# Kernel tuning notes

Measured on AMD Instinct MI355X. Metric: run time of the kernel, lower is better.

Reference implementation:

```python
import jax, jax.numpy as jnp
import numpy as np

N_NODES = 100000
N_EDGES = 400000
IN_DIM, HID, OUT_DIM, NUM_REL = 768, 256, 128, 3


def _init_linear(key, fan_in, fan_out):
    k1, k2 = jax.random.split(key)
    s = 1.0 / np.sqrt(fan_in)
    W = jax.random.uniform(k1, (fan_in, fan_out), jnp.float32, -s, s)
    b = jax.random.uniform(k2, (fan_out,), jnp.float32, -s, s)
    return W, b


def setup_inputs() -> dict:
    key = jax.random.key(0)
    ks = jax.random.split(key, 12)
    x = jax.random.normal(ks[0], (N_NODES, IN_DIM), jnp.float32)
    edge_index = jax.random.randint(ks[1], (2, N_EDGES), 0, N_NODES, jnp.int64 if jax.config.jax_enable_x64 else jnp.int32).astype(jnp.int32)
    edge_type = jax.random.randint(ks[2], (N_EDGES,), 0, NUM_REL).astype(jnp.int32)
    W1, b1 = _init_linear(ks[3], IN_DIM, HID)
    s = 1.0 / np.sqrt(HID)
    conv1_W = jax.random.uniform(ks[4], (NUM_REL, HID, HID), jnp.float32, -s, s)
    conv1_root = jax.random.uniform(ks[5], (HID, HID), jnp.float32, -s, s)
    conv1_bias = jnp.zeros((HID,), jnp.float32)
    conv2_W = jax.random.uniform(ks[6], (NUM_REL, HID, HID), jnp.float32, -s, s)
    conv2_root = jax.random.uniform(ks[7], (HID, HID), jnp.float32, -s, s)
    conv2_bias = jnp.zeros((HID,), jnp.float32)
    W2, b2 = _init_linear(ks[8], HID, OUT_DIM)
    Wc, bc = _init_linear(ks[9], OUT_DIM, 2)
    return {"x": x, "edge_index": edge_index, "edge_type": edge_type,
            "batch_size": 1024,
            "W1": W1, "b1": b1,
            "conv1_W": conv1_W, "conv1_root": conv1_root, "conv1_bias": conv1_bias,
            "conv2_W": conv2_W, "conv2_root": conv2_root, "conv2_bias": conv2_bias,
            "W2": W2, "b2": b2, "Wc": Wc, "bc": bc}


def rgcn_conv(h, src, dst, edge_type, W, root, bias):
    # PyG RGCNConv: mean aggregation per relation + root transform + bias
    n = h.shape[0]
    hs = h[src]                                   # [E, HID] gather
    out = h @ root + bias                         # root/self term
    for r in range(NUM_REL):                      # fixed small relation count
        w = (edge_type == r).astype(h.dtype)      # [E]
        msg = (hs @ W[r]) * w[:, None]            # per-relation transform
        ssum = jax.ops.segment_sum(msg, dst, num_segments=n)
        cnt = jax.ops.segment_sum(w, dst, num_segments=n)
        out = out + ssum / jnp.maximum(cnt, 1.0)[:, None]
    return out


def reference(x, edge_index, edge_type, batch_size,
              W1, b1, conv1_W, conv1_root, conv1_bias,
              conv2_W, conv2_root, conv2_bias, W2, b2, Wc, bc):
    src, dst = edge_index[0], edge_index[1]
    h = jax.nn.relu(x @ W1 + b1)                  # linear1 + ReLU
    h = rgcn_conv(h, src, dst, edge_type, conv1_W, conv1_root, conv1_bias)
    # dropout: identity at inference
    h = rgcn_conv(h, src, dst, edge_type, conv2_W, conv2_root, conv2_bias)
    h = jax.nn.relu(h @ W2 + b2)                  # linear2 + ReLU
    logits = h @ Wc + bc                          # classifier
    return logits[:batch_size]
```

## Files before the change

kernel.cpp:

```cpp
#include <hip/hip_runtime.h>


#define N_NODES 100000
#define N_EDGES 400000
#define IN_DIM  768
#define HID     256
#define OUT_DIM 128
#define NREL    3
#define BATCH   1024
#define KCAT    1024
#define MSGW    768
#define CAP0    32768
#define CAP1    8192
#define ECAP1   32768
#define ECAP2   8192

typedef __attribute__((ext_vector_type(8))) short bf16x8;
typedef __attribute__((ext_vector_type(4))) float f32x4;

static __device__ __forceinline__ int imin(int a, int b) { return a < b ? a : b; }

static __device__ __forceinline__ unsigned short f2bf(float f) {
    union { float f; unsigned int u; } v; v.f = f;
    unsigned int r = v.u + 0x7FFFu + ((v.u >> 16) & 1u);
    return (unsigned short)(r >> 16);
}

#define P1n  ((IN_DIM * HID) / 8)
#define P2n  ((KCAT * HID) / 8)
#define PW2n ((HID * OUT_DIM) / 8)

__global__ __launch_bounds__(256) void prep_mark1(
    uint4* __restrict__ zp, int nzA,
    const float* __restrict__ W1,
    const float* __restrict__ c1root, const float* __restrict__ c1W,
    const float* __restrict__ c2root, const float* __restrict__ c2W,
    const float* __restrict__ W2,
    unsigned short* __restrict__ w1s,
    unsigned short* __restrict__ B1s,
    unsigned short* __restrict__ B2s,
    unsigned short* __restrict__ W2t,
    const int* __restrict__ ei, int* __restrict__ need1,
    int* __restrict__ elist2, int* __restrict__ ectr2)
{
    int t = blockIdx.x * blockDim.x + threadIdx.x;
    if (t < nzA) { zp[t] = make_uint4(0u, 0u, 0u, 0u); return; }
    int u = t - nzA;
    if (u < P1n) {
        int base = u * 8;
        int j0 = base & 31, c = (base >> 5) & 255, s = base >> 13;
        unsigned int pk[4];
        #pragma unroll
        for (int q = 0; q < 4; q++) {
            unsigned short lo = f2bf(W1[((s * 32 + j0 + 2 * q) << 8) + c]);
            unsigned short hi = f2bf(W1[((s * 32 + j0 + 2 * q + 1) << 8) + c]);
            pk[q] = (unsigned int)lo | ((unsigned int)hi << 16);
        }
        *(uint4*)&w1s[base] = make_uint4(pk[0], pk[1], pk[2], pk[3]);
        return;
    }
    u -= P1n;
    if (u < 2 * P2n) {
        int which2 = u >= P2n;
        const float* root = which2 ? c2root : c1root;
        const float* Wr   = which2 ? c2W : c1W;
        unsigned short* dst = which2 ? B2s : B1s;
        int base = (u - (which2 ? P2n : 0)) * 8;
        int j0 = base & 31, c = (base >> 5) & 255, s = base >> 13;
        int k0 = s * 32 + j0;
        unsigned int pk[4];
        #pragma unroll
        for (int q = 0; q < 4; q++) {
            int ka = k0 + 2 * q, kb = ka + 1;
            float va = (ka < HID) ? root[(ka << 8) + c] : Wr[((ka - HID) << 8) + c];
            float vb = (kb < HID) ? root[(kb << 8) + c] : Wr[((kb - HID) << 8) + c];
            pk[q] = (unsigned int)f2bf(va) | ((unsigned int)f2bf(vb) << 16);
        }
        *(uint4*)&dst[base] = make_uint4(pk[0], pk[1], pk[2], pk[3]);
        return;
    }
    u -= 2 * P2n;
    if (u < PW2n) {
        int s = u >> 9, f = (u >> 6) & 7, l = u & 63;
        int kb = s * 32 + ((l >> 4) << 3);
        int c  = (f << 4) + (l & 15);
        unsigned int pk[4];
        #pragma unroll
        for (int q = 0; q < 4; q++) {
            unsigned short lo = f2bf(W2[(size_t)(kb + 2 * q)     * OUT_DIM + c]);
            unsigned short hi = f2bf(W2[(size_t)(kb + 2 * q + 1) * OUT_DIM + c]);
            pk[q] = (unsigned int)lo | ((unsigned int)hi << 16);
        }
        *(uint4*)&W2t[(size_t)u * 8] = make_uint4(pk[0], pk[1], pk[2], pk[3]);
        return;
    }
    u -= PW2n;
    if (u < N_EDGES) {
        if (ei[N_EDGES + u] < BATCH) {
            need1[ei[u]] = 1;
            int p = atomicAdd(ectr2, 1);
            if (p < ECAP2) elist2[p] = u;
        }
    }
}

__global__ void mark0_compact1(const int* __restrict__ ei, const int* __restrict__ need1,
                               int* __restrict__ need0,
                               int* __restrict__ elist1, int* __restrict__ ectr1,
                               int* __restrict__ idx1, int* __restrict__ map1,
                               int* __restrict__ n1ctr) {
    int t = blockIdx.x * blockDim.x + threadIdx.x;
    if (t < N_EDGES) {
        int d = ei[N_EDGES + t];
        if (d < BATCH || need1[d]) {
            need0[ei[t]] = 1;
            int p = atomicAdd(ectr1, 1);
            if (p < ECAP1) elist1[p] = t;
        }
        return;
    }
    int i = t - N_EDGES;
    if (i < N_NODES) {
        if ((i < BATCH) | need1[i]) {
            int p = atomicAdd(n1ctr, 1);
            if (p < CAP1) { idx1[p] = i; map1[i] = p; } else map1[i] = -1;
        } else map1[i] = -1;
    }
}

__global__ void compact0(const int* __restrict__ map1, const int* __restrict__ need0,
                         int* __restrict__ idx0, int* __restrict__ map0,
                         int* __restrict__ n0ctr) {
    int i = blockIdx.x * blockDim.x + threadIdx.x;
    if (i >= N_NODES) return;
    if ((map1[i] >= 0) | need0[i]) {
        int p = atomicAdd(n0ctr, 1);
        if (p < CAP0) { idx0[p] = i; map0[i] = p; } else map0[i] = -1;
    } else map0[i] = -1;
}

__global__ void scatter_c(const int* __restrict__ ei, const int* __restrict__ et,
                          const int* __restrict__ elist, const int* __restrict__ ectr, int ecap,
                          const int* __restrict__ mapSrc, const int* __restrict__ mapDst,
                          const float* __restrict__ hsrc,
                          float* __restrict__ Amsg, float* __restrict__ cnt,
                          int cntStride) {
    int g = blockIdx.x * blockDim.x + threadIdx.x;
    int ii = g >> 6, lane = g & 63;
    int n = imin(*ectr, ecap);
    if (ii >= n) return;
    int e = elist[ii];
    int d = ei[N_EDGES + e];
    int row = mapDst ? mapDst[d] : d;
    if (row < 0) return;
    int s = mapSrc[ei[e]];
    if (s < 0) return;
    int r = et[e];
    float4 v = *(const float4*)(hsrc + (size_t)s * HID + lane * 4);
    float* dp = Amsg + (size_t)row * MSGW + (size_t)r * HID + lane * 4;
    atomicAdd(dp + 0, v.x);
    atomicAdd(dp + 1, v.y);
    atomicAdd(dp + 2, v.z);
    atomicAdd(dp + 3, v.w);
    if (lane == 0) atomicAdd(cnt + (size_t)r * cntStride + row, 1.0f);
}

__global__ __launch_bounds__(256) void gemm1_mfma(
    const float* __restrict__ x, const int* __restrict__ idx0,
    const unsigned short* __restrict__ w1s, const float* __restrict__ b1,
    float* __restrict__ h0c, const int* __restrict__ Mptr, int Mcap)
{
    int M = imin(*Mptr, Mcap);
    int bm = blockIdx.x * 64;
    if (bm >= M) return;

    __shared__ unsigned short As[64][40];
    __shared__ unsigned short Bs[256][40];

    int tid = threadIdx.x;
    int w = tid >> 6, lane = tid & 63;
    int l16 = lane & 15, lhi = lane >> 4;

    int ar = tid >> 2, ac = tid & 3;
    int gr = idx0[imin(bm + ar, M - 1)];
    const float* aptr = x + (size_t)gr * IN_DIM + ac * 8;

    f32x4 acc[16];
    #pragma unroll
    for (int i = 0; i < 16; i++) acc[i] = (f32x4)0.0f;

    for (int k0 = 0; k0 < IN_DIM; k0 += 32) {
        float4 a0 = *(const float4*)(aptr + k0);
        float4 a1 = *(const float4*)(aptr + k0 + 4);
        unsigned int p0 = (unsigned int)f2bf(a0.x) | ((unsigned int)f2bf(a0.y) << 16);
        unsigned int p1 = (unsigned int)f2bf(a0.z) | ((unsigned int)f2bf(a0.w) << 16);
        unsigned int p2 = (unsigned int)f2bf(a1.x) | ((unsigned int)f2bf(a1.y) << 16);
        unsigned int p3 = (unsigned int)f2bf(a1.z) | ((unsigned int)f2bf(a1.w) << 16);
        *(uint4*)&As[ar][ac * 8] = make_uint4(p0, p1, p2, p3);

        const uint4* bsrc = (const uint4*)(w1s + ((size_t)(k0 >> 5) * 256 + tid) * 32);
        int bswz = (tid >> 3) & 3;
        uint4 b0 = bsrc[0], b1v = bsrc[1], b2 = bsrc[2], b3 = bsrc[3];
        *(uint4*)&Bs[tid][(0 ^ bswz) * 8] = b0;
        *(uint4*)&Bs[tid][(1 ^ bswz) * 8] = b1v;
        *(uint4*)&Bs[tid][(2 ^ bswz) * 8] = b2;
        *(uint4*)&Bs[tid][(3 ^ bswz) * 8] = b3;
        __syncthreads();

        bf16x8 af = *(bf16x8*)&As[w * 16 + l16][lhi * 8];
        #pragma unroll
        for (int f = 0; f < 16; f++) {
            int col = f * 16 + l16;
            bf16x8 bf = *(bf16x8*)&Bs[col][(lhi ^ ((col >> 3) & 3)) * 8];
            acc[f] = __builtin_amdgcn_mfma_f32_16x16x32_bf16(af, bf, acc[f], 0, 0, 0);
        }
        __syncthreads();
    }

    #pragma unroll
    for (int f = 0; f < 16; f++) {
        int col = f * 16 + l16;
        float bb = b1[col];
        #pragma unroll
        for (int reg = 0; reg < 4; reg++) {
            int row = bm + w * 16 + lhi * 4 + reg;
            if (row < M) h0c[(size_t)row * HID + col] = fmaxf(acc[f][reg] + bb, 0.0f);
        }
    }
}

__global__ __launch_bounds__(256) void conv_mfma(
    const float* __restrict__ hsrc,
    const int* __restrict__ idx, const int* __restrict__ map,
    const float* __restrict__ Amsg,
    const float* __restrict__ cnt, int cntStride,
    const unsigned short* __restrict__ Bt, const float* __restrict__ bias,
    float* __restrict__ Cout, const int* __restrict__ Mptr, int Mcap)
{
    int M = Mptr ? imin(*Mptr, Mcap) : Mcap;
    int bm = blockIdx.x * 64;
    if (bm >= M) return;

    __shared__ unsigned short As[64][40];
    __shared__ unsigned short Bs[256][40];

    int tid = threadIdx.x;
    int w = tid >> 6, lane = tid & 63;
    int l16 = lane & 15, lhi = lane >> 4;

    int ar = tid >> 2, ac = tid & 3;
    int row = imin(bm + ar, M - 1);
    int node = idx ? idx[row] : row;
    int grow = map[node]; if (grow < 0) grow = 0;
    const float* rootp = hsrc + (size_t)grow * HID + ac * 8;
    const float* msgp  = Amsg + (size_t)row * MSGW + ac * 8;
    float sc[NREL];
    #pragma unroll
    for (int r = 0; r < NREL; r++)
        sc[r] = 1.0f / fmaxf(cnt[(size_t)r * cntStride + row], 1.0f);

    f32x4 acc[16];
    #pragma unroll
    for (int i = 0; i < 16; i++) acc[i] = (f32x4)0.0f;

    for (int k0 = 0; k0 < KCAT; k0 += 32) {
        float4 a0, a1;
        if (k0 < HID) {
            a0 = *(const float4*)(rootp + k0);
            a1 = *(const float4*)(rootp + k0 + 4);
        } else {
            float s = sc[(k0 - HID) >> 8];
            a0 = *(const float4*)(msgp + (k0 - HID));
            a1 = *(const float4*)(msgp + (k0 - HID) + 4);
            a0.x *= s; a0.y *= s; a0.z *= s; a0.w *= s;
            a1.x *= s; a1.y *= s; a1.z *= s; a1.w *= s;
        }
        unsigned int p0 = (unsigned int)f2bf(a0.x) | ((unsigned int)f2bf(a0.y) << 16);
        unsigned int p1 = (unsigned int)f2bf(a0.z) | ((unsigned int)f2bf(a0.w) << 16);
        unsigned int p2 = (unsigned int)f2bf(a1.x) | ((unsigned int)f2bf(a1.y) << 16);
        unsigned int p3 = (unsigned int)f2bf(a1.z) | ((unsigned int)f2bf(a1.w) << 16);
        *(uint4*)&As[ar][ac * 8] = make_uint4(p0, p1, p2, p3);

        const uint4* bsrc = (const uint4*)(Bt + ((size_t)(k0 >> 5) * 256 + tid) * 32);
        int bswz = (tid >> 3) & 3;
        uint4 b0 = bsrc[0], b1v = bsrc[1], b2 = bsrc[2], b3 = bsrc[3];
        *(uint4*)&Bs[tid][(0 ^ bswz) * 8] = b0;
        *(uint4*)&Bs[tid][(1 ^ bswz) * 8] = b1v;
        *(uint4*)&Bs[tid][(2 ^ bswz) * 8] = b2;
        *(uint4*)&Bs[tid][(3 ^ bswz) * 8] = b3;
        __syncthreads();

        bf16x8 af = *(bf16x8*)&As[w * 16 + l16][lhi * 8];
        #pragma unroll
        for (int f = 0; f < 16; f++) {
            int col = f * 16 + l16;
            bf16x8 bf = *(bf16x8*)&Bs[col][(lhi ^ ((col >> 3) & 3)) * 8];
            acc[f] = __builtin_amdgcn_mfma_f32_16x16x32_bf16(af, bf, acc[f], 0, 0, 0);
        }
        __syncthreads();
    }

    #pragma unroll
    for (int f = 0; f < 16; f++) {
        int col = f * 16 + l16;
        float bb = bias[col];
        #pragma unroll
        for (int reg = 0; reg < 4; reg++) {
            int r = bm + w * 16 + lhi * 4 + reg;
            if (r < M) Cout[(size_t)r * HID + col] = acc[f][reg] + bb;
        }
    }
}

__global__ __launch_bounds__(256) void conv2_fused(
    const float* __restrict__ hsrc, const int* __restrict__ map,
    const float* __restrict__ Amsg, const float* __restrict__ cnt,
    const unsigned short* __restrict__ Bt, const float* __restrict__ c2bias,
    const unsigned short* __restrict__ W2t, const float* __restrict__ b2,
    const float* __restrict__ Wc, const float* __restrict__ bc,
    float* __restrict__ out)
{
    int bm = blockIdx.x * 64;

    __shared__ unsigned short As[64][40];
    __shared__ unsigned short Bs[256][40];
    __shared__ unsigned short h2s[64][264];

    int tid = threadIdx.x;
    int w = tid >> 6, lane = tid & 63;
    int l16 = lane & 15, lhi = lane >> 4;

    int ar = tid >> 2, ac = tid & 3;
    int row = bm + ar;
    int grow = map[row]; if (grow < 0) grow = 0;
    const float* rootp = hsrc + (size_t)grow * HID + ac * 8;
    const float* msgp  = Amsg + (size_t)row * MSGW + ac * 8;
    float sc[NREL];
    #pragma unroll
    for (int r = 0; r < NREL; r++)
        sc[r] = 1.0f / fmaxf(cnt[(size_t)r * BATCH + row], 1.0f);

    f32x4 acc[16];
    #pragma unroll
    for (int i = 0; i < 16; i++) acc[i] = (f32x4)0.0f;

    for (int k0 = 0; k0 < KCAT; k0 += 32) {
        float4 a0, a1;
        if (k0 < HID) {
            a0 = *(const float4*)(rootp + k0);
            a1 = *(const float4*)(rootp + k0 + 4);
        } else {
            float s = sc[(k0 - HID) >> 8];
            a0 = *(const float4*)(msgp + (k0 - HID));
            a1 = *(const float4*)(msgp + (k0 - HID) + 4);
            a0.x *= s; a0.y *= s; a0.z *= s; a0.w *= s;
            a1.x *= s; a1.y *= s; a1.z *= s; a1.w *= s;
        }
        unsigned int p0 = (unsigned int)f2bf(a0.x) | ((unsigned int)f2bf(a0.y) << 16);
        unsigned int p1 = (unsigned int)f2bf(a0.z) | ((unsigned int)f2bf(a0.w) << 16);
        unsigned int p2 = (unsigned int)f2bf(a1.x) | ((unsigned int)f2bf(a1.y) << 16);
        unsigned int p3 = (unsigned int)f2bf(a1.z) | ((unsigned int)f2bf(a1.w) << 16);
        *(uint4*)&As[ar][ac * 8] = make_uint4(p0, p1, p2, p3);

        const uint4* bsrc = (const uint4*)(Bt + ((size_t)(k0 >> 5) * 256 + tid) * 32);
        int bswz = (tid >> 3) & 3;
        uint4 b0 = bsrc[0], b1v = bsrc[1], b2v = bsrc[2], b3 = bsrc[3];
        *(uint4*)&Bs[tid][(0 ^ bswz) * 8] = b0;
        *(uint4*)&Bs[tid][(1 ^ bswz) * 8] = b1v;
        *(uint4*)&Bs[tid][(2 ^ bswz) * 8] = b2v;
        *(uint4*)&Bs[tid][(3 ^ bswz) * 8] = b3;
        __syncthreads();

        bf16x8 af = *(bf16x8*)&As[w * 16 + l16][lhi * 8];
        #pragma unroll
        for (int f = 0; f < 16; f++) {
            int col = f * 16 + l16;
            bf16x8 bf = *(bf16x8*)&Bs[col][(lhi ^ ((col >> 3) & 3)) * 8];
            acc[f] = __builtin_amdgcn_mfma_f32_16x16x32_bf16(af, bf, acc[f], 0, 0, 0);
        }
        __syncthreads();
    }

    #pragma unroll
    for (int f = 0; f < 16; f++) {
        int col = f * 16 + l16;
        float bb = c2bias[col];
        #pragma unroll
        for (int reg = 0; reg < 4; reg++)
            h2s[w * 16 + lhi * 4 + reg][col] = f2bf(acc[f][reg] + bb);
    }
    __syncthreads();

    f32x4 acc2[8];
    #pragma unroll
    for (int i = 0; i < 8; i++) acc2[i] = (f32x4)0.0f;
    for (int s = 0; s < 8; s++) {
        bf16x8 af = *(bf16x8*)&h2s[w * 16 + l16][s * 32 + lhi * 8];
        #pragma unroll
        for (int f = 0; f < 8; f++) {
            bf16x8 bf = *(const bf16x8*)(W2t + ((size_t)(s * 8 + f) * 64 + lane) * 8);
            acc2[f] = __builtin_amdgcn_mfma_f32_16x16x32_bf16(af, bf, acc2[f], 0, 0, 0);
        }
    }

    float p0[4] = {0.f, 0.f, 0.f, 0.f}, p1[4] = {0.f, 0.f, 0.f, 0.f};
    #pragma unroll
    for (int f = 0; f < 8; f++) {
        int col = f * 16 + l16;
        float w0 = Wc[col * 2 + 0], w1 = Wc[col * 2 + 1];
        float bb = b2[col];
        #pragma unroll
        for (int reg = 0; reg < 4; reg++) {
            float h = fmaxf(acc2[f][reg] + bb, 0.0f);
            p0[reg] += h * w0;
            p1[reg] += h * w1;
        }
    }
    #pragma unroll
    for (int o = 1; o <= 8; o <<= 1) {
        #pragma unroll
        for (int reg = 0; reg < 4; reg++) {
            p0[reg] += __shfl_xor(p0[reg], o);
            p1[reg] += __shfl_xor(p1[reg], o);
        }
    }
    if (l16 == 0) {
        #pragma unroll
        for (int reg = 0; reg < 4; reg++) {
            int r = bm + w * 16 + lhi * 4 + reg;
            out[r * 2 + 0] = p0[reg] + bc[0];
            out[r * 2 + 1] = p1[reg] + bc[1];
        }
    }
}


extern "C" void kernel_launch(void* const* d_in, const int* in_sizes, int n_in,
                              void* d_out, int out_size, void* d_ws, size_t ws_size,
                              hipStream_t stream) {
    const float* x      = (const float*)d_in[0];
    const int*   ei     = (const int*)d_in[1];
    const int*   et     = (const int*)d_in[2];
    const float* W1     = (const float*)d_in[4];
    const float* b1     = (const float*)d_in[5];
    const float* c1W    = (const float*)d_in[6];
    const float* c1root = (const float*)d_in[7];
    const float* c1bias = (const float*)d_in[8];
    const float* c2W    = (const float*)d_in[9];
    const float* c2root = (const float*)d_in[10];
    const float* c2bias = (const float*)d_in[11];
    const float* W2     = (const float*)d_in[12];
    const float* b2     = (const float*)d_in[13];
    const float* Wc     = (const float*)d_in[14];
    const float* bc     = (const float*)d_in[15];
    float* out = (float*)d_out;

    char* ws = (char*)d_ws;
    size_t off = 0;
    auto alloc = [&](size_t bytes) -> char* {
        char* p = ws + off;
        off = (off + bytes + 255) & ~(size_t)255;
        return p;
    };

    size_t zb_ctr  = 16;
    size_t zb_cnt1 = (size_t)NREL * CAP1 * 4;
    size_t zb_cnt2 = (size_t)NREL * BATCH * 4;
    size_t zb_need = (size_t)N_NODES * 4;
    size_t msbytes = zb_ctr + zb_cnt1 + zb_cnt2 + 2 * zb_need;
    char* zsmall = alloc(msbytes);
    int*   n1ctr = (int*)zsmall;
    int*   n0ctr = n1ctr + 1;
    int*   ectr1 = n1ctr + 2;
    int*   ectr2 = n1ctr + 3;
    float* cnt1  = (float*)(zsmall + zb_ctr);
    float* cnt2  = (float*)(zsmall + zb_ctr + zb_cnt1);
    int*   need1 = (int*)(zsmall + zb_ctr + zb_cnt1 + zb_cnt2);
    int*   need0 = (int*)((char*)need1 + zb_need);

    size_t zb_amsg1 = (size_t)CAP1 * MSGW * 4;
    size_t zb_amsg2 = (size_t)BATCH * MSGW * 4;
    char* amsg = alloc(zb_amsg1 + zb_amsg2);
    float* Amsg1 = (float*)amsg;
    float* Amsg2 = (float*)(amsg + zb_amsg1);
    int nzA = (int)((zb_amsg1 + zb_amsg2) / 16);

    int* map1  = (int*)alloc(N_NODES * 4);
    int* map0  = (int*)alloc(N_NODES * 4);
    int* idx1  = (int*)alloc(CAP1 * 4);
    int* idx0  = (int*)alloc(CAP0 * 4);
    int* elist1 = (int*)alloc(ECAP1 * 4);
    int* elist2 = (int*)alloc(ECAP2 * 4);
    float* h0c = (float*)alloc((size_t)CAP0 * HID * 4);
    float* h1c = (float*)alloc((size_t)CAP1 * HID * 4);
    unsigned short* w1s = (unsigned short*)alloc((size_t)IN_DIM * HID * 2);
    unsigned short* B1s = (unsigned short*)alloc((size_t)KCAT * HID * 2);
    unsigned short* B2s = (unsigned short*)alloc((size_t)KCAT * HID * 2);
    unsigned short* W2t = (unsigned short*)alloc((size_t)HID * OUT_DIM * 2);
    (void)ws_size; (void)in_sizes; (void)n_in; (void)out_size;

    const int NB = 256;

    hipMemsetAsync(zsmall, 0, msbytes, stream);
    int n1_total = nzA + P1n + 2 * P2n + PW2n + N_EDGES;
    prep_mark1<<<dim3((n1_total + NB - 1) / NB), NB, 0, stream>>>(
        (uint4*)amsg, nzA, W1, c1root, c1W, c2root, c2W, W2,
        w1s, B1s, B2s, W2t, ei, need1, elist2, ectr2);
    int n2_total = N_EDGES + N_NODES;
    mark0_compact1<<<dim3((n2_total + NB - 1) / NB), NB, 0, stream>>>(
        ei, need1, need0, elist1, ectr1, idx1, map1, n1ctr);
    compact0<<<dim3((N_NODES + NB - 1) / NB), NB, 0, stream>>>(map1, need0, idx0, map0, n0ctr);
    gemm1_mfma<<<dim3(CAP0 / 64), NB, 0, stream>>>(x, idx0, w1s, b1, h0c, n0ctr, CAP0);
    scatter_c<<<dim3(ECAP1 * 64 / NB), NB, 0, stream>>>(ei, et, elist1, ectr1, ECAP1,
                                                        map0, map1, h0c, Amsg1, cnt1, CAP1);
    conv_mfma<<<dim3(CAP1 / 64), NB, 0, stream>>>(h0c, idx1, map0, Amsg1, cnt1, CAP1,
                                                  B1s, c1bias, h1c, n1ctr, CAP1);
    scatter_c<<<dim3(ECAP2 * 64 / NB), NB, 0, stream>>>(ei, et, elist2, ectr2, ECAP2,
                                                        map1, nullptr, h1c, Amsg2, cnt2, BATCH);
    conv2_fused<<<dim3(BATCH / 64), NB, 0, stream>>>(h1c, map1, Amsg2, cnt2,
                                                     B2s, c2bias, W2t, b2, Wc, bc, out);
}
```

Before: 379.4 us.

## Fuse layer-2 scatter into conv1 epilogue via per-tile edge buckets

```diff
diff --git a/kernel.cpp b/kernel.cpp
--- a/kernel.cpp
+++ b/kernel.cpp
@@ -14,6 +14,8 @@
 #define CAP1    8192
 #define ECAP1   32768
 #define ECAP2   8192
+#define NTILE1  (CAP1 / 64)
+#define BKT2CAP 512
 
 typedef __attribute__((ext_vector_type(8))) short bf16x8;
 typedef __attribute__((ext_vector_type(4))) float f32x4;
@@ -26,12 +28,17 @@
     return (unsigned short)(r >> 16);
 }
 
+static __device__ __forceinline__ float bf2f(unsigned short h) {
+    union { unsigned int u; float f; } c; c.u = ((unsigned int)h) << 16;
+    return c.f;
+}
+
 #define P1n  ((IN_DIM * HID) / 8)
 #define P2n  ((KCAT * HID) / 8)
 #define PW2n ((HID * OUT_DIM) / 8)
 
 __global__ __launch_bounds__(256) void prep_mark1(
-    uint4* __restrict__ zp, int nzA,
+    uint4* __restrict__ zp, int nzA2,
     const float* __restrict__ W1,
     const float* __restrict__ c1root, const float* __restrict__ c1W,
     const float* __restrict__ c2root, const float* __restrict__ c2W,
@@ -44,8 +51,13 @@
     int* __restrict__ elist2, int* __restrict__ ectr2)
 {
     int t = blockIdx.x * blockDim.x + threadIdx.x;
-    if (t < nzA) { zp[t] = make_uint4(0u, 0u, 0u, 0u); return; }
-    int u = t - nzA;
+    if (t < nzA2) {
+        uint4 z = make_uint4(0u, 0u, 0u, 0u);
+        zp[2 * t] = z;
+        zp[2 * t + 1] = z;
+        return;
+    }
+    int u = t - nzA2;
     if (u < P1n) {
         int base = u * 8;
         int j0 = base & 31, c = (base >> 5) & 255, s = base >> 13;
@@ -128,41 +140,59 @@
     }
 }
 
-__global__ void compact0(const int* __restrict__ map1, const int* __restrict__ need0,
-                         int* __restrict__ idx0, int* __restrict__ map0,
-                         int* __restrict__ n0ctr) {
-    int i = blockIdx.x * blockDim.x + threadIdx.x;
-    if (i >= N_NODES) return;
-    if ((map1[i] >= 0) | need0[i]) {
-        int p = atomicAdd(n0ctr, 1);
-        if (p < CAP0) { idx0[p] = i; map0[i] = p; } else map0[i] = -1;
-    } else map0[i] = -1;
-}
-
-__global__ void scatter_c(const int* __restrict__ ei, const int* __restrict__ et,
-                          const int* __restrict__ elist, const int* __restrict__ ectr, int ecap,
-                          const int* __restrict__ mapSrc, const int* __restrict__ mapDst,
-                          const float* __restrict__ hsrc,
-                          float* __restrict__ Amsg, float* __restrict__ cnt,
-                          int cntStride) {
-    int g = blockIdx.x * blockDim.x + threadIdx.x;
-    int ii = g >> 6, lane = g & 63;
+__global__ void compact0_bucket(const int* __restrict__ map1, const int* __restrict__ need0,
+                                int* __restrict__ idx0, int* __restrict__ map0,
+                                int* __restrict__ n0ctr,
+                                const int* __restrict__ ei,
+                                const int* __restrict__ elist2, const int* __restrict__ ectr2,
+                                int* __restrict__ bkt2cnt, int* __restrict__ bkt2) {
+    int t = blockIdx.x * blockDim.x + threadIdx.x;
+    if (t < N_NODES) {
+        if ((map1[t] >= 0) | need0[t]) {
+            int p = atomicAdd(n0ctr, 1);
+            if (p < CAP0) { idx0[p] = t; map0[t] = p; } else map0[t] = -1;
+        } else map0[t] = -1;
+        return;
+    }
+    int j = t - N_NODES;
+    int n2 = imin(*ectr2, ECAP2);
+    if (j < n2) {
+        int e = elist2[j];
+        int r = map1[ei[e]];
+        if (r >= 0) {
+            int tile = r >> 6;
+            int p = atomicAdd(&bkt2cnt[tile], 1);
+            if (p < BKT2CAP) bkt2[tile * BKT2CAP + p] = e;
+        }
+    }
+}
+
+__global__ void scatter_gs(const int* __restrict__ ei, const int* __restrict__ et,
+                           const int* __restrict__ elist, const int* __restrict__ ectr, int ecap,
+                           const int* __restrict__ mapSrc, const int* __restrict__ mapDst,
+                           const float* __restrict__ hsrc,
+                           float* __restrict__ Amsg, float* __restrict__ cnt,
+                           int cntStride) {
     int n = imin(*ectr, ecap);
-    if (ii >= n) return;
-    int e = elist[ii];
-    int d = ei[N_EDGES + e];
-    int row = mapDst ? mapDst[d] : d;
-    if (row < 0) return;
-    int s = mapSrc[ei[e]];
-    if (s < 0) return;
-    int r = et[e];
-    float4 v = *(const float4*)(hsrc + (size_t)s * HID + lane * 4);
-    float* dp = Amsg + (size_t)row * MSGW + (size_t)r * HID + lane * 4;
-    atomicAdd(dp + 0, v.x);
-    atomicAdd(dp + 1, v.y);
-    atomicAdd(dp + 2, v.z);
-    atomicAdd(dp + 3, v.w);
-    if (lane == 0) atomicAdd(cnt + (size_t)r * cntStride + row, 1.0f);
+    int tot = n * 64;
+    int gstr = gridDim.x * blockDim.x;
+    for (int g = blockIdx.x * blockDim.x + threadIdx.x; g < tot; g += gstr) {
+        int ii = g >> 6, lane = g & 63;
+        int e = elist[ii];
+        int d = ei[N_EDGES + e];
+        int row = mapDst ? mapDst[d] : d;
+        if (row < 0) continue;
+        int s = mapSrc[ei[e]];
+        if (s < 0) continue;
+        int r = et[e];
+        float4 v = *(const float4*)(hsrc + (size_t)s * HID + lane * 4);
+        float* dp = Amsg + (size_t)row * MSGW + (size_t)r * HID + lane * 4;
+        atomicAdd(dp + 0, v.x);
+        atomicAdd(dp + 1, v.y);
+        atomicAdd(dp + 2, v.z);
+        atomicAdd(dp + 3, v.w);
+        if (lane == 0) atomicAdd(cnt + (size_t)r * cntStride + row, 1.0f);
+    }
 }
 
 __global__ __launch_bounds__(256) void gemm1_mfma(
@@ -229,20 +259,25 @@
     }
 }
 
-__global__ __launch_bounds__(256) void conv_mfma(
+__global__ __launch_bounds__(256) void conv1_scat(
     const float* __restrict__ hsrc,
-    const int* __restrict__ idx, const int* __restrict__ map,
-    const float* __restrict__ Amsg,
-    const float* __restrict__ cnt, int cntStride,
+    const int* __restrict__ idx1, const int* __restrict__ map0,
+    const int* __restrict__ map1,
+    const float* __restrict__ Amsg, const float* __restrict__ cnt, int cntStride,
     const unsigned short* __restrict__ Bt, const float* __restrict__ bias,
-    float* __restrict__ Cout, const int* __restrict__ Mptr, int Mcap)
+    float* __restrict__ Cout, const int* __restrict__ Mptr, int Mcap,
+    const int* __restrict__ ei, const int* __restrict__ et,
+    const int* __restrict__ bkt2cnt, const int* __restrict__ bkt2,
+    float* __restrict__ Amsg2, float* __restrict__ cnt2)
 {
-    int M = Mptr ? imin(*Mptr, Mcap) : Mcap;
+    int M = imin(*Mptr, Mcap);
     int bm = blockIdx.x * 64;
     if (bm >= M) return;
 
-    __shared__ unsigned short As[64][40];
-    __shared__ unsigned short Bs[256][40];
+    __shared__ __align__(16) char smem[64 * 264 * 2];
+    unsigned short (*As)[40]   = (unsigned short(*)[40])smem;
+    unsigned short (*Bs)[40]   = (unsigned short(*)[40])(smem + 64 * 40 * 2);
+    unsigned short (*h1s)[264] = (unsigned short(*)[264])smem;
 
     int tid = threadIdx.x;
     int w = tid >> 6, lane = tid & 63;
@@ -250,8 +285,8 @@
 
     int ar = tid >> 2, ac = tid & 3;
     int row = imin(bm + ar, M - 1);
-    int node = idx ? idx[row] : row;
-    int grow = map[node]; if (grow < 0) grow = 0;
+    int node = idx1[row];
+    int grow = map0[node]; if (grow < 0) grow = 0;
     const float* rootp = hsrc + (size_t)grow * HID + ac * 8;
     const float* msgp  = Amsg + (size_t)row * MSGW + ac * 8;
     float sc[NREL];
@@ -283,10 +318,10 @@
 
         const uint4* bsrc = (const uint4*)(Bt + ((size_t)(k0 >> 5) * 256 + tid) * 32);
         int bswz = (tid >> 3) & 3;
-        uint4 b0 = bsrc[0], b1v = bsrc[1], b2 = bsrc[2], b3 = bsrc[3];
+        uint4 b0 = bsrc[0], b1v = bsrc[1], b2v = bsrc[2], b3 = bsrc[3];
         *(uint4*)&Bs[tid][(0 ^ bswz) * 8] = b0;
         *(uint4*)&Bs[tid][(1 ^ bswz) * 8] = b1v;
-        *(uint4*)&Bs[tid][(2 ^ bswz) * 8] = b2;
+        *(uint4*)&Bs[tid][(2 ^ bswz) * 8] = b2v;
         *(uint4*)&Bs[tid][(3 ^ bswz) * 8] = b3;
         __syncthreads();
 
@@ -306,9 +341,30 @@
         float bb = bias[col];
         #pragma unroll
         for (int reg = 0; reg < 4; reg++) {
-            int r = bm + w * 16 + lhi * 4 + reg;
-            if (r < M) Cout[(size_t)r * HID + col] = acc[f][reg] + bb;
-        }
+            int rr = w * 16 + lhi * 4 + reg;
+            float v = acc[f][reg] + bb;
+            if (bm + rr < M) Cout[(size_t)(bm + rr) * HID + col] = v;
+            h1s[rr][col] = f2bf(v);
+        }
+    }
+    __syncthreads();
+
+    int nb = imin(bkt2cnt[blockIdx.x], BKT2CAP);
+    for (int ii = w; ii < nb; ii += 4) {
+        int e = bkt2[blockIdx.x * BKT2CAP + ii];
+        int dst = ei[N_EDGES + e];
+        int r = map1[ei[e]] - bm;
+        int rel = et[e];
+        float v0 = bf2f(h1s[r][lane * 4 + 0]);
+        float v1 = bf2f(h1s[r][lane * 4 + 1]);
+        float v2 = bf2f(h1s[r][lane * 4 + 2]);
+        float v3 = bf2f(h1s[r][lane * 4 + 3]);
+        float* dp = Amsg2 + (size_t)dst * MSGW + (size_t)rel * HID + lane * 4;
+        atomicAdd(dp + 0, v0);
+        atomicAdd(dp + 1, v1);
+        atomicAdd(dp + 2, v2);
+        atomicAdd(dp + 3, v3);
+        if (lane == 0) atomicAdd(&cnt2[(size_t)rel * BATCH + dst], 1.0f);
     }
 }
 
@@ -464,26 +520,28 @@
     };
 
     size_t zb_ctr  = 16;
+    size_t zb_bkt  = (size_t)NTILE1 * 4;
     size_t zb_cnt1 = (size_t)NREL * CAP1 * 4;
     size_t zb_cnt2 = (size_t)NREL * BATCH * 4;
     size_t zb_need = (size_t)N_NODES * 4;
-    size_t msbytes = zb_ctr + zb_cnt1 + zb_cnt2 + 2 * zb_need;
+    size_t msbytes = zb_ctr + zb_bkt + zb_cnt1 + zb_cnt2 + 2 * zb_need;
     char* zsmall = alloc(msbytes);
-    int*   n1ctr = (int*)zsmall;
-    int*   n0ctr = n1ctr + 1;
-    int*   ectr1 = n1ctr + 2;
-    int*   ectr2 = n1ctr + 3;
-    float* cnt1  = (float*)(zsmall + zb_ctr);
-    float* cnt2  = (float*)(zsmall + zb_ctr + zb_cnt1);
-    int*   need1 = (int*)(zsmall + zb_ctr + zb_cnt1 + zb_cnt2);
-    int*   need0 = (int*)((char*)need1 + zb_need);
+    int*   n1ctr   = (int*)zsmall;
+    int*   n0ctr   = n1ctr + 1;
+    int*   ectr1   = n1ctr + 2;
+    int*   ectr2   = n1ctr + 3;
+    int*   bkt2cnt = (int*)(zsmall + zb_ctr);
+    float* cnt1    = (float*)(zsmall + zb_ctr + zb_bkt);
+    float* cnt2    = (float*)(zsmall + zb_ctr + zb_bkt + zb_cnt1);
+    int*   need1   = (int*)(zsmall + zb_ctr + zb_bkt + zb_cnt1 + zb_cnt2);
+    int*   need0   = (int*)((char*)need1 + zb_need);
 
     size_t zb_amsg1 = (size_t)CAP1 * MSGW * 4;
     size_t zb_amsg2 = (size_t)BATCH * MSGW * 4;
     char* amsg = alloc(zb_amsg1 + zb_amsg2);
     float* Amsg1 = (float*)amsg;
     float* Amsg2 = (float*)(amsg + zb_amsg1);
-    int nzA = (int)((zb_amsg1 + zb_amsg2) / 16);
+    int nzA2 = (int)((zb_amsg1 + zb_amsg2) / 32);
 
     int* map1  = (int*)alloc(N_NODES * 4);
     int* map0  = (int*)alloc(N_NODES * 4);
@@ -491,6 +549,7 @@
     int* idx0  = (int*)alloc(CAP0 * 4);
     int* elist1 = (int*)alloc(ECAP1 * 4);
     int* elist2 = (int*)alloc(ECAP2 * 4);
+    int* bkt2   = (int*)alloc((size_t)NTILE1 * BKT2CAP * 4);
     float* h0c = (float*)alloc((size_t)CAP0 * HID * 4);
     float* h1c = (float*)alloc((size_t)CAP1 * HID * 4);
     unsigned short* w1s = (unsigned short*)alloc((size_t)IN_DIM * HID * 2);
@@ -502,21 +561,22 @@
     const int NB = 256;
 
     hipMemsetAsync(zsmall, 0, msbytes, stream);
-    int n1_total = nzA + P1n + 2 * P2n + PW2n + N_EDGES;
+    int n1_total = nzA2 + P1n + 2 * P2n + PW2n + N_EDGES;
     prep_mark1<<<dim3((n1_total + NB - 1) / NB), NB, 0, stream>>>(
-        (uint4*)amsg, nzA, W1, c1root, c1W, c2root, c2W, W2,
+        (uint4*)amsg, nzA2, W1, c1root, c1W, c2root, c2W, W2,
         w1s, B1s, B2s, W2t, ei, need1, elist2, ectr2);
     int n2_total = N_EDGES + N_NODES;
     mark0_compact1<<<dim3((n2_total + NB - 1) / NB), NB, 0, stream>>>(
         ei, need1, need0, elist1, ectr1, idx1, map1, n1ctr);
-    compact0<<<dim3((N_NODES + NB - 1) / NB), NB, 0, stream>>>(map1, need0, idx0, map0, n0ctr);
+    int n3_total = N_NODES + ECAP2;
+    compact0_bucket<<<dim3((n3_total + NB - 1) / NB), NB, 0, stream>>>(
+        map1, need0, idx0, map0, n0ctr, ei, elist2, ectr2, bkt2cnt, bkt2);
     gemm1_mfma<<<dim3(CAP0 / 64), NB, 0, stream>>>(x, idx0, w1s, b1, h0c, n0ctr, CAP0);
-    scatter_c<<<dim3(ECAP1 * 64 / NB), NB, 0, stream>>>(ei, et, elist1, ectr1, ECAP1,
-                                                        map0, map1, h0c, Amsg1, cnt1, CAP1);
-    conv_mfma<<<dim3(CAP1 / 64), NB, 0, stream>>>(h0c, idx1, map0, Amsg1, cnt1, CAP1,
-                                                  B1s, c1bias, h1c, n1ctr, CAP1);
-    scatter_c<<<dim3(ECAP2 * 64 / NB), NB, 0, stream>>>(ei, et, elist2, ectr2, ECAP2,
-                                                        map1, nullptr, h1c, Amsg2, cnt2, BATCH);
+    scatter_gs<<<dim3(2048), NB, 0, stream>>>(ei, et, elist1, ectr1, ECAP1,
+                                              map0, map1, h0c, Amsg1, cnt1, CAP1);
+    conv1_scat<<<dim3(CAP1 / 64), NB, 0, stream>>>(
+        h0c, idx1, map0, map1, Amsg1, cnt1, CAP1, B1s, c1bias, h1c, n1ctr, CAP1,
+        ei, et, bkt2cnt, bkt2, Amsg2, cnt2);
     conv2_fused<<<dim3(BATCH / 64), NB, 0, stream>>>(h1c, map1, Amsg2, cnt2,
                                                      B2s, c2bias, W2t, b2, Wc, bc, out);
 }
```

After: 385.1 us, median of 2. Within noise of the previous version (+1.5%).
